# Optimization experiments

Hardware: AMD Instinct MI355X
Metric: run time of the kernel (lower is better)

Reference implementation:

```python
import jax, jax.numpy as jnp
import numpy as np
import math

B, N, D, H, FFN = 4, 2048, 512, 8, 2048
DK = D // H
EPS = 1e-5


def _layer_norm(x, g, b):
    mu = jnp.mean(x, axis=-1, keepdims=True)
    var = jnp.mean((x - mu) ** 2, axis=-1, keepdims=True)
    return (x - mu) * jax.lax.rsqrt(var + EPS) * g + b


def _rotate_half(x):
    h = x.shape[-1] // 2
    return jnp.concatenate([-x[..., h:], x[..., :h]], axis=-1)


def _rope(q, k, positions):
    # q, k: (B, H, N, DK); positions: (B, N) int
    inv_freq = 1.0 / (10000.0 ** (jnp.arange(0, DK, 2, dtype=jnp.float32) / DK))  # (DK/2,)
    ang = positions[:, None, :, None].astype(jnp.float32) * inv_freq  # (B,1,N,DK/2)
    cos = jnp.concatenate([jnp.cos(ang), jnp.cos(ang)], axis=-1)  # (B,1,N,DK)
    sin = jnp.concatenate([jnp.sin(ang), jnp.sin(ang)], axis=-1)
    q = q * cos + _rotate_half(q) * sin
    k = k * cos + _rotate_half(k) * sin
    return q, k


def setup_inputs() -> dict:
    key = jax.random.key(0)
    ks = jax.random.split(key, 16)
    s = 0.02
    x = jax.random.normal(ks[0], (B, N, D), dtype=jnp.float32)
    # backward-looking hop mask within jobs: random boolean with True diagonal
    m = jax.random.uniform(ks[1], (B, N, N)) < 0.1
    o2o_mask = m | jnp.eye(N, dtype=bool)[None]
    positions = jax.random.randint(ks[2], (B, N), 0, N)
    params = {
        'wq': jax.random.normal(ks[3], (D, D)) * s, 'bq': jnp.zeros((D,)),
        'wk': jax.random.normal(ks[4], (D, D)) * s, 'bk': jnp.zeros((D,)),
        'wv': jax.random.normal(ks[5], (D, D)) * s, 'bv': jnp.zeros((D,)),
        'wo': jax.random.normal(ks[6], (D, D)) * s, 'bo': jnp.zeros((D,)),
        'ln1_g': jnp.ones((D,)), 'ln1_b': jnp.zeros((D,)),
        'ln2_g': jnp.ones((D,)), 'ln2_b': jnp.zeros((D,)),
        'w1': jax.random.normal(ks[7], (D, FFN)) * s, 'b1': jnp.zeros((FFN,)),
        'w2': jax.random.normal(ks[8], (FFN, D)) * s, 'b2': jnp.zeros((D,)),
    }
    return {'x': x, 'o2o_mask': o2o_mask, 'positions': positions, **params}


def reference(x, o2o_mask, positions, wq, bq, wk, bk, wv, bv, wo, bo,
              ln1_g, ln1_b, ln2_g, ln2_b, w1, b1, w2, b2):
    residual = x
    xn = _layer_norm(x, ln1_g, ln1_b)
    q = (xn @ wq + bq).reshape(B, N, H, DK).transpose(0, 2, 1, 3)
    k = (xn @ wk + bk).reshape(B, N, H, DK).transpose(0, 2, 1, 3)
    v = (xn @ wv + bv).reshape(B, N, H, DK).transpose(0, 2, 1, 3)
    q, k = _rope(q, k, positions)
    scores = jnp.einsum('bhqd,bhkd->bhqk', q, k) / math.sqrt(DK)
    scores = jnp.where(o2o_mask[:, None], scores, -jnp.inf)
    attn = jax.nn.softmax(scores, axis=-1)
    attn = jnp.where(jnp.isnan(attn), 0.0, attn)  # fully-masked rows -> 0
    attn_out = jnp.einsum('bhqk,bhkd->bhqd', attn, v)
    attn_out = attn_out.transpose(0, 2, 1, 3).reshape(B, N, D)
    x = residual + (attn_out @ wo + bo)
    residual = x
    h = _layer_norm(x, ln2_g, ln2_b)
    h = jax.nn.relu(h @ w1 + b1) @ w2 + b2
    return residual + h
```

## Files before the change

kernel.cpp:

```cpp
#include <hip/hip_runtime.h>
#include <hip/hip_bf16.h>

typedef __attribute__((ext_vector_type(8))) __bf16 bf16x8;
typedef __attribute__((ext_vector_type(4))) __bf16 bf16x4;
typedef __attribute__((ext_vector_type(4))) float f32x4;

#define B_ 4
#define N_ 2048
#define D_ 512
#define H_ 8
#define DK_ 64
#define F_ 2048

__device__ __forceinline__ void async16(const __bf16* g, __bf16* l) {
  __builtin_amdgcn_global_load_lds((const __attribute__((address_space(1))) void*)g,
                                   (__attribute__((address_space(3))) void*)l, 16, 0, 0);
}

__global__ __launch_bounds__(256) void transpose_w(const float* __restrict__ in,
                                                   __bf16* __restrict__ out,
                                                   int K, int Nc) {
  __shared__ float t[64][65];
  const int k0 = blockIdx.x * 64, n0 = blockIdx.y * 64;
  const int c = threadIdx.x & 63, r4 = threadIdx.x >> 6;
#pragma unroll
  for (int p = 0; p < 16; p++) {
    int rr = p * 4 + r4;
    t[rr][c] = in[(size_t)(k0 + rr) * Nc + n0 + c];
  }
  __syncthreads();
#pragma unroll
  for (int p = 0; p < 16; p++) {
    int rr = p * 4 + r4;
    out[(size_t)(n0 + rr) * K + k0 + c] = (__bf16)t[c][rr];
  }
}

__global__ void concat_bias(const float* __restrict__ bq, const float* __restrict__ bk,
                            const float* __restrict__ bv, float* __restrict__ o) {
  int i = blockIdx.x * 256 + threadIdx.x;
  o[i] = (i < 512) ? bq[i] : (i < 1024) ? bk[i - 512] : bv[i - 1024];
}

__global__ __launch_bounds__(256) void build_bitmask(const int* __restrict__ mask,
                                                     unsigned long long* __restrict__ bm) {
  size_t t = (size_t)blockIdx.x * 256 + threadIdx.x;
  int m = mask[t];
  unsigned long long w = __ballot(m != 0);
  if ((threadIdx.x & 63) == 0) bm[t >> 6] = w;
}

__global__ __launch_bounds__(256) void ln_fwd(const float* __restrict__ x,
                                              const float* __restrict__ g,
                                              const float* __restrict__ b,
                                              __bf16* __restrict__ out) {
  int row = blockIdx.x * 4 + (threadIdx.x >> 6);
  int lane = threadIdx.x & 63;
  const float* xr = x + (size_t)row * D_ + lane * 8;
  float4 a0 = *(const float4*)xr;
  float4 a1 = *(const float4*)(xr + 4);
  float v[8] = {a0.x, a0.y, a0.z, a0.w, a1.x, a1.y, a1.z, a1.w};
  float s = 0.f;
#pragma unroll
  for (int i = 0; i < 8; i++) s += v[i];
#pragma unroll
  for (int off = 1; off < 64; off <<= 1) s += __shfl_xor(s, off);
  float mu = s * (1.f / D_);
  float q = 0.f;
#pragma unroll
  for (int i = 0; i < 8; i++) { float d = v[i] - mu; q += d * d; }
#pragma unroll
  for (int off = 1; off < 64; off <<= 1) q += __shfl_xor(q, off);
  float rs = rsqrtf(q * (1.f / D_) + 1e-5f);
  const float* gp = g + lane * 8;
  const float* bp = b + lane * 8;
  alignas(16) __bf16 o[8];
#pragma unroll
  for (int i = 0; i < 8; i++) o[i] = (__bf16)((v[i] - mu) * rs * gp[i] + bp[i]);
  *(bf16x8*)(out + (size_t)row * D_ + lane * 8) = *(bf16x8*)o;
}

__global__ __launch_bounds__(256) void rope_qk(const __bf16* __restrict__ qkv,
                                               const int* __restrict__ pos,
                                               __bf16* __restrict__ qo,
                                               __bf16* __restrict__ ko) {
  int t = blockIdx.x * 256 + threadIdx.x;
  int d = t & 31;
  int h = (t >> 5) & 7;
  int n = (t >> 8) & (N_ - 1);
  int b = t >> 19;
  const __bf16* base = qkv + (size_t)(b * N_ + n) * 1536 + h * 64 + d;
  float q1 = (float)base[0], q2 = (float)base[32];
  float k1 = (float)base[512], k2 = (float)base[544];
  float p = (float)pos[b * N_ + n];
  float inv = __expf(-(float)d * (9.210340371976184f / 32.f));
  float ang = p * inv;
  float sn, cs;
  sincosf(ang, &sn, &cs);
  size_t ob = ((size_t)(b * H_ + h) * N_ + n) * DK_ + d;
  qo[ob]      = (__bf16)(q1 * cs - q2 * sn);
  qo[ob + 32] = (__bf16)(q2 * cs + q1 * sn);
  ko[ob]      = (__bf16)(k1 * cs - k2 * sn);
  ko[ob + 32] = (__bf16)(k2 * cs + k1 * sn);
}

__global__ __launch_bounds__(256) void v_trans(const __bf16* __restrict__ qkv,
                                               __bf16* __restrict__ vt) {
  __shared__ __bf16 t[64][65];
  int n0 = blockIdx.x * 64, h = blockIdx.y, b = blockIdx.z;
  int c = threadIdx.x & 63, rr = threadIdx.x >> 6;
#pragma unroll
  for (int p = 0; p < 16; p++) {
    int i = p * 4 + rr;
    t[i][c] = qkv[(size_t)(b * N_ + n0 + i) * 1536 + 1024 + h * 64 + c];
  }
  __syncthreads();
  size_t ob = (size_t)(b * H_ + h) * DK_ * N_;
#pragma unroll
  for (int p = 0; p < 16; p++) {
    int dd = p * 4 + rr;
    vt[ob + (size_t)dd * N_ + n0 + c] = t[c][dd];
  }
}

template <int RELU, int OBF, int RES>
__global__ __launch_bounds__(256) void gemm_bt(const __bf16* __restrict__ A,
                                               const __bf16* __restrict__ Bt,
                                               const float* __restrict__ bias,
                                               const float* __restrict__ res,
                                               void* __restrict__ Cout,
                                               int M, int N, int K) {
  __shared__ __bf16 As[128 * 32];
  __shared__ __bf16 Bs[128 * 32];
  const int tid = threadIdx.x;
  const int lane = tid & 63;
  const int wave = tid >> 6;
  const int quad = lane >> 4;
  const int l16 = lane & 15;
  const int m0 = blockIdx.y * 128;
  const int n0 = blockIdx.x * 128;
  const int wm = (wave >> 1) * 64;
  const int wn = (wave & 1) * 64;
  f32x4 acc[4][4] = {};

  const int c0 = tid, c1 = tid + 256;
  const int ar0 = c0 >> 2, ak0 = (c0 & 3) * 8;
  const int ar1 = c1 >> 2, ak1 = (c1 & 3) * 8;

  for (int k0 = 0; k0 < K; k0 += 32) {
    async16(A + (size_t)(m0 + ar0) * K + k0 + ak0, As + c0 * 8);
    async16(A + (size_t)(m0 + ar1) * K + k0 + ak1, As + c1 * 8);
    async16(Bt + (size_t)(n0 + ar0) * K + k0 + ak0, Bs + c0 * 8);
    async16(Bt + (size_t)(n0 + ar1) * K + k0 + ak1, Bs + c1 * 8);
    __syncthreads();
    bf16x8 af[4], bf[4];
#pragma unroll
    for (int mi = 0; mi < 4; mi++)
      af[mi] = *(const bf16x8*)(As + (wm + mi * 16 + l16) * 32 + quad * 8);
#pragma unroll
    for (int ni = 0; ni < 4; ni++)
      bf[ni] = *(const bf16x8*)(Bs + (wn + ni * 16 + l16) * 32 + quad * 8);
#pragma unroll
    for (int mi = 0; mi < 4; mi++)
#pragma unroll
      for (int ni = 0; ni < 4; ni++)
        acc[mi][ni] = __builtin_amdgcn_mfma_f32_16x16x32_bf16(af[mi], bf[ni], acc[mi][ni], 0, 0, 0);
    __syncthreads();
  }
#pragma unroll
  for (int ni = 0; ni < 4; ni++) {
    const int col = n0 + wn + ni * 16 + l16;
    const float bv = bias[col];
#pragma unroll
    for (int mi = 0; mi < 4; mi++) {
#pragma unroll
      for (int r = 0; r < 4; r++) {
        const int row = m0 + wm + mi * 16 + quad * 4 + r;
        float v = acc[mi][ni][r] + bv;
        if (RES) v += res[(size_t)row * N + col];
        if (RELU) v = fmaxf(v, 0.f);
        if (OBF) ((__bf16*)Cout)[(size_t)row * N + col] = (__bf16)v;
        else     ((float*)Cout)[(size_t)row * N + col] = v;
      }
    }
  }
}

template <int RELU, int OBF, int RES>
__global__ __launch_bounds__(256) void gemm_bt64(const __bf16* __restrict__ A,
                                                 const __bf16* __restrict__ Bt,
                                                 const float* __restrict__ bias,
                                                 const float* __restrict__ res,
                                                 void* __restrict__ Cout,
                                                 int M, int N, int K) {
  __shared__ __bf16 As[128 * 32];
  __shared__ __bf16 Bs[64 * 32];
  const int tid = threadIdx.x;
  const int lane = tid & 63;
  const int wave = tid >> 6;
  const int quad = lane >> 4;
  const int l16 = lane & 15;
  const int m0 = blockIdx.y * 128;
  const int n0 = blockIdx.x * 64;
  const int wm = wave * 32;
  f32x4 acc[2][4] = {};

  const int ar0 = tid >> 2, ak0 = (tid & 3) * 8;

  for (int k0 = 0; k0 < K; k0 += 32) {
    async16(A + (size_t)(m0 + ar0) * K + k0 + ak0, As + tid * 8);
    async16(A + (size_t)(m0 + 64 + ar0) * K + k0 + ak0, As + (tid + 256) * 8);
    async16(Bt + (size_t)(n0 + ar0) * K + k0 + ak0, Bs + tid * 8);
    __syncthreads();
    bf16x8 af[2], bf[4];
#pragma unroll
    for (int mi = 0; mi < 2; mi++)
      af[mi] = *(const bf16x8*)(As + (wm + mi * 16 + l16) * 32 + quad * 8);
#pragma unroll
    for (int ni = 0; ni < 4; ni++)
      bf[ni] = *(const bf16x8*)(Bs + (ni * 16 + l16) * 32 + quad * 8);
#pragma unroll
    for (int mi = 0; mi < 2; mi++)
#pragma unroll
      for (int ni = 0; ni < 4; ni++)
        acc[mi][ni] = __builtin_amdgcn_mfma_f32_16x16x32_bf16(af[mi], bf[ni], acc[mi][ni], 0, 0, 0);
    __syncthreads();
  }
#pragma unroll
  for (int ni = 0; ni < 4; ni++) {
    const int col = n0 + ni * 16 + l16;
    const float bv = bias[col];
#pragma unroll
    for (int mi = 0; mi < 2; mi++) {
#pragma unroll
      for (int r = 0; r < 4; r++) {
        const int row = m0 + wm + mi * 16 + quad * 4 + r;
        float v = acc[mi][ni][r] + bv;
        if (RES) v += res[(size_t)row * N + col];
        if (RELU) v = fmaxf(v, 0.f);
        if (OBF) ((__bf16*)Cout)[(size_t)row * N + col] = (__bf16)v;
        else     ((float*)Cout)[(size_t)row * N + col] = v;
      }
    }
  }
}

__global__ __launch_bounds__(256, 2) void flash_attn(const __bf16* __restrict__ q,
                                                     const __bf16* __restrict__ k,
                                                     const __bf16* __restrict__ vt,
                                                     const unsigned long long* __restrict__ bm,
                                                     __bf16* __restrict__ out) {
  const int qt = blockIdx.x, h = blockIdx.y, b = blockIdx.z;
  const int tid = threadIdx.x;
  const int lane = tid & 63, wave = tid >> 6;
  const int quad = lane >> 4, l16 = lane & 15;
  __shared__ __bf16 Ks[2][64 * 64];
  __shared__ __bf16 Vs[2][64 * 64];
  __shared__ __bf16 P[4][2][16 * 68];
  const size_t bh = (size_t)b * H_ + h;
  const __bf16* qp = q + (bh * N_ + qt * 128 + wave * 32) * DK_;
  bf16x8 qf[2][2];
#pragma unroll
  for (int s = 0; s < 2; s++)
#pragma unroll
    for (int ks = 0; ks < 2; ks++) {
      qf[s][ks] = *(const bf16x8*)(qp + (s * 16 + l16) * DK_ + ks * 32 + quad * 8);
#pragma unroll
      for (int j = 0; j < 8; j++) qf[s][ks][j] = qf[s][ks][j] * (__bf16)0.125f;
    }
  const __bf16* kbase = k + bh * N_ * DK_;
  const __bf16* vbase = vt + bh * DK_ * N_;
  const int qrow0 = qt * 128 + wave * 32 + l16;
  const unsigned long long* bmr0 = bm + (size_t)(b * N_ + qrow0) * (N_ / 64);
  const unsigned long long* bmr1 = bmr0 + 16 * (N_ / 64);
  const int xo = l16 & 7;

  f32x4 oacc[2][4] = {};
  float lsum[2] = {0.f, 0.f};

  auto stage = [&](int kt, int buf) {
    const __bf16* kg = kbase + (size_t)kt * 64 * DK_;
    const __bf16* vg = vbase + kt * 64;
#pragma unroll
    for (int i = 0; i < 2; i++) {
      const int s = tid + i * 256;
      const int r = s >> 3;
      const int j = (s & 7) ^ (r & 7);
      async16(kg + r * DK_ + j * 8, Ks[buf] + s * 8);
      async16(vg + (size_t)r * N_ + j * 8, Vs[buf] + s * 8);
    }
  };

  stage(0, 0);
  __syncthreads();

  for (int kt = 0; kt < N_ / 64; kt++) {
    const int buf = kt & 1;
    if (kt + 1 < N_ / 64) stage(kt + 1, buf ^ 1);

    const unsigned long long mw0 = bmr0[kt] >> (quad * 4);
    const unsigned long long mw1 = bmr1[kt] >> (quad * 4);
#pragma unroll
    for (int ci = 0; ci < 4; ci++) {
      const int row = ci * 16 + l16;
      bf16x8 kf0 = *(const bf16x8*)(Ks[buf] + (row * 8 + (quad ^ xo)) * 8);
      bf16x8 kf1 = *(const bf16x8*)(Ks[buf] + (row * 8 + ((4 + quad) ^ xo)) * 8);
#pragma unroll
      for (int s = 0; s < 2; s++) {
        f32x4 a = {0.f, 0.f, 0.f, 0.f};
        a = __builtin_amdgcn_mfma_f32_16x16x32_bf16(kf0, qf[s][0], a, 0, 0, 0);
        a = __builtin_amdgcn_mfma_f32_16x16x32_bf16(kf1, qf[s][1], a, 0, 0, 0);
        const unsigned long long mw = s ? mw1 : mw0;
        bf16x4 pk;
#pragma unroll
        for (int r = 0; r < 4; r++) {
          float in = ((mw >> (ci * 16 + r)) & 1ull) ? a[r] : -1e30f;
          float p = __expf(in);
          lsum[s] += p;
          pk[r] = (__bf16)p;
        }
        *(bf16x4*)(&P[wave][s][0] + l16 * 68 + ci * 16 + quad * 4) = pk;
      }
    }
    bf16x8 pf[2][2];
#pragma unroll
    for (int s = 0; s < 2; s++) {
      pf[s][0] = *(const bf16x8*)(&P[wave][s][0] + l16 * 68 + quad * 8);
      pf[s][1] = *(const bf16x8*)(&P[wave][s][0] + l16 * 68 + 32 + quad * 8);
    }
#pragma unroll
    for (int ni = 0; ni < 4; ni++) {
      const int row = ni * 16 + l16;
      bf16x8 vf0 = *(const bf16x8*)(Vs[buf] + (row * 8 + (quad ^ xo)) * 8);
      bf16x8 vf1 = *(const bf16x8*)(Vs[buf] + (row * 8 + ((4 + quad) ^ xo)) * 8);
#pragma unroll
      for (int s = 0; s < 2; s++) {
        oacc[s][ni] = __builtin_amdgcn_mfma_f32_16x16x32_bf16(vf0, pf[s][0], oacc[s][ni], 0, 0, 0);
        oacc[s][ni] = __builtin_amdgcn_mfma_f32_16x16x32_bf16(vf1, pf[s][1], oacc[s][ni], 0, 0, 0);
      }
    }
    __syncthreads();
  }
#pragma unroll
  for (int s = 0; s < 2; s++) {
    lsum[s] += __shfl_xor(lsum[s], 16);
    lsum[s] += __shfl_xor(lsum[s], 32);
    const float inv_l = (lsum[s] > 0.f) ? 1.f / lsum[s] : 0.f;
#pragma unroll
    for (int ni = 0; ni < 4; ni++) {
      bf16x4 ov;
#pragma unroll
      for (int r = 0; r < 4; r++) ov[r] = (__bf16)(oacc[s][ni][r] * inv_l);
      *(bf16x4*)(out + ((size_t)b * N_ + qrow0 + s * 16) * D_ + h * DK_ + ni * 16 + quad * 4) = ov;
    }
  }
}

static constexpr size_t OFF_XN  = 0;
static constexpr size_t OFF_WT  = 8388608;
static constexpr size_t OFF_WO  = OFF_WT + 1572864;
static constexpr size_t OFF_W1  = OFF_WO + 524288;
static constexpr size_t OFF_W2  = OFF_W1 + 2097152;
static constexpr size_t OFF_BQ  = OFF_W2 + 2097152;
static constexpr size_t OFF_QKV = OFF_BQ + 6144;
static constexpr size_t OFF_QR  = OFF_QKV + 25165824;
static constexpr size_t OFF_KR  = OFF_QR + 8388608;
static constexpr size_t OFF_VT  = OFF_KR + 8388608;
static constexpr size_t OFF_AO  = OFF_VT + 8388608;
static constexpr size_t OFF_Y   = OFF_AO + 8388608;

extern "C" void kernel_launch(void* const* d_in, const int* in_sizes, int n_in,
                              void* d_out, int out_size, void* d_ws, size_t ws_size,
                              hipStream_t stream) {
  const float* x    = (const float*)d_in[0];
  const int*   mask = (const int*)d_in[1];
  const int*   pos  = (const int*)d_in[2];
  const float* wq   = (const float*)d_in[3];
  const float* bq   = (const float*)d_in[4];
  const float* wk   = (const float*)d_in[5];
  const float* bk   = (const float*)d_in[6];
  const float* wv   = (const float*)d_in[7];
  const float* bv   = (const float*)d_in[8];
  const float* wo   = (const float*)d_in[9];
  const float* bo   = (const float*)d_in[10];
  const float* ln1g = (const float*)d_in[11];
  const float* ln1b = (const float*)d_in[12];
  const float* ln2g = (const float*)d_in[13];
  const float* ln2b = (const float*)d_in[14];
  const float* w1   = (const float*)d_in[15];
  const float* b1   = (const float*)d_in[16];
  const float* w2   = (const float*)d_in[17];
  const float* b2   = (const float*)d_in[18];
  float* out = (float*)d_out;
  char* ws = (char*)d_ws;

  __bf16* xn    = (__bf16*)(ws + OFF_XN);
  __bf16* wqkvt = (__bf16*)(ws + OFF_WT);
  __bf16* wot   = (__bf16*)(ws + OFF_WO);
  __bf16* w1t   = (__bf16*)(ws + OFF_W1);
  __bf16* w2t   = (__bf16*)(ws + OFF_W2);
  float*  bqkv  = (float*)(ws + OFF_BQ);
  __bf16* qkv   = (__bf16*)(ws + OFF_QKV);
  __bf16* qr    = (__bf16*)(ws + OFF_QR);
  __bf16* kr    = (__bf16*)(ws + OFF_KR);
  __bf16* vt    = (__bf16*)(ws + OFF_VT);
  __bf16* attn  = (__bf16*)(ws + OFF_AO);
  float*  y     = (float*)(ws + OFF_Y);
  unsigned long long* bm = (unsigned long long*)(ws + OFF_Y);
  __bf16* hn    = xn;
  __bf16* h2    = qkv;

  dim3 b256(256);
  transpose_w<<<dim3(8, 8), b256, 0, stream>>>(wq, wqkvt, 512, 512);
  transpose_w<<<dim3(8, 8), b256, 0, stream>>>(wk, wqkvt + 512 * 512, 512, 512);
  transpose_w<<<dim3(8, 8), b256, 0, stream>>>(wv, wqkvt + 1024 * 512, 512, 512);
  transpose_w<<<dim3(8, 8), b256, 0, stream>>>(wo, wot, 512, 512);
  transpose_w<<<dim3(8, 32), b256, 0, stream>>>(w1, w1t, 512, 2048);
  transpose_w<<<dim3(32, 8), b256, 0, stream>>>(w2, w2t, 2048, 512);
  concat_bias<<<6, b256, 0, stream>>>(bq, bk, bv, bqkv);
  build_bitmask<<<65536, b256, 0, stream>>>(mask, bm);

  ln_fwd<<<2048, b256, 0, stream>>>(x, ln1g, ln1b, xn);
  gemm_bt<0, 1, 0><<<dim3(12, 64), b256, 0, stream>>>(xn, wqkvt, bqkv, nullptr, qkv, 8192, 1536, 512);
  rope_qk<<<8192, b256, 0, stream>>>(qkv, pos, qr, kr);
  v_trans<<<dim3(32, 8, 4), b256, 0, stream>>>(qkv, vt);

  flash_attn<<<dim3(16, 8, 4), b256, 0, stream>>>(qr, kr, vt, bm, attn);

  gemm_bt64<0, 0, 1><<<dim3(8, 64), b256, 0, stream>>>(attn, wot, bo, x, y, 8192, 512, 512);
  ln_fwd<<<2048, b256, 0, stream>>>(y, ln2g, ln2b, hn);
  gemm_bt<1, 1, 0><<<dim3(16, 64), b256, 0, stream>>>(hn, w1t, b1, nullptr, h2, 8192, 2048, 512);
  gemm_bt64<0, 0, 1><<<dim3(8, 64), b256, 0, stream>>>(h2, w2t, b2, y, out, 8192, 512, 2048);
}
```

Measured before the change: 391.4 us.

## Split attention KV range in two with combine kernel and MFMA row sums

New measurement: 417.6 us. 1.07x slower.

```diff
diff --git a/kernel.cpp b/kernel.cpp
--- a/kernel.cpp
+++ b/kernel.cpp
@@ -1,5 +1,6 @@
 #include <hip/hip_runtime.h>
 #include <hip/hip_bf16.h>
+#include <math.h>
 
 typedef __attribute__((ext_vector_type(8))) __bf16 bf16x8;
 typedef __attribute__((ext_vector_type(4))) __bf16 bf16x4;
@@ -245,12 +246,14 @@
   }
 }
 
-__global__ __launch_bounds__(256, 2) void flash_attn(const __bf16* __restrict__ q,
+__global__ __launch_bounds__(256, 3) void flash_attn(const __bf16* __restrict__ q,
                                                      const __bf16* __restrict__ k,
                                                      const __bf16* __restrict__ vt,
                                                      const unsigned long long* __restrict__ bm,
-                                                     __bf16* __restrict__ out) {
-  const int qt = blockIdx.x, h = blockIdx.y, b = blockIdx.z;
+                                                     __bf16* __restrict__ po,
+                                                     float* __restrict__ lsg) {
+  const int qt = blockIdx.x, h = blockIdx.y;
+  const int b = blockIdx.z >> 1, half = blockIdx.z & 1;
   const int tid = threadIdx.x;
   const int lane = tid & 63, wave = tid >> 6;
   const int quad = lane >> 4, l16 = lane & 15;
@@ -259,15 +262,20 @@
   __shared__ __bf16 P[4][2][16 * 68];
   const size_t bh = (size_t)b * H_ + h;
   const __bf16* qp = q + (bh * N_ + qt * 128 + wave * 32) * DK_;
+  const float qscale = 0.125f * 1.44269504f;
   bf16x8 qf[2][2];
 #pragma unroll
   for (int s = 0; s < 2; s++)
 #pragma unroll
     for (int ks = 0; ks < 2; ks++) {
-      qf[s][ks] = *(const bf16x8*)(qp + (s * 16 + l16) * DK_ + ks * 32 + quad * 8);
-#pragma unroll
-      for (int j = 0; j < 8; j++) qf[s][ks][j] = qf[s][ks][j] * (__bf16)0.125f;
-    }
+      bf16x8 raw = *(const bf16x8*)(qp + (s * 16 + l16) * DK_ + ks * 32 + quad * 8);
+#pragma unroll
+      for (int j = 0; j < 8; j++) qf[s][ks][j] = (__bf16)((float)raw[j] * qscale);
+    }
+  bf16x8 onesf;
+#pragma unroll
+  for (int j = 0; j < 8; j++) onesf[j] = (__bf16)1.0f;
+
   const __bf16* kbase = k + bh * N_ * DK_;
   const __bf16* vbase = vt + bh * DK_ * N_;
   const int qrow0 = qt * 128 + wave * 32 + l16;
@@ -275,8 +283,19 @@
   const unsigned long long* bmr1 = bmr0 + 16 * (N_ / 64);
   const int xo = l16 & 7;
 
+  const __bf16* kA[2], * kB[2], * vA[2], * vB[2];
+#pragma unroll
+  for (int bf = 0; bf < 2; bf++) {
+    kA[bf] = Ks[bf] + (l16 * 8 + (quad ^ xo)) * 8;
+    kB[bf] = Ks[bf] + (l16 * 8 + ((4 + quad) ^ xo)) * 8;
+    vA[bf] = Vs[bf] + (l16 * 8 + (quad ^ xo)) * 8;
+    vB[bf] = Vs[bf] + (l16 * 8 + ((4 + quad) ^ xo)) * 8;
+  }
+  __bf16* Pw[2] = {&P[wave][0][0] + l16 * 68 + quad * 4, &P[wave][1][0] + l16 * 68 + quad * 4};
+  const __bf16* Pr[2] = {&P[wave][0][0] + l16 * 68 + quad * 8, &P[wave][1][0] + l16 * 68 + quad * 8};
+
   f32x4 oacc[2][4] = {};
-  float lsum[2] = {0.f, 0.f};
+  f32x4 lacc[2] = {};
 
   auto stage = [&](int kt, int buf) {
     const __bf16* kg = kbase + (size_t)kt * 64 * DK_;
@@ -291,48 +310,53 @@
     }
   };
 
-  stage(0, 0);
+  const int kt0 = half * 16;
+  stage(kt0, 0);
+  unsigned long long nm0 = bmr0[kt0], nm1 = bmr1[kt0];
   __syncthreads();
 
-  for (int kt = 0; kt < N_ / 64; kt++) {
-    const int buf = kt & 1;
-    if (kt + 1 < N_ / 64) stage(kt + 1, buf ^ 1);
-
-    const unsigned long long mw0 = bmr0[kt] >> (quad * 4);
-    const unsigned long long mw1 = bmr1[kt] >> (quad * 4);
+  for (int it = 0; it < 16; it++) {
+    const int kt = kt0 + it;
+    const int buf = it & 1;
+    if (it + 1 < 16) stage(kt + 1, buf ^ 1);
+    const unsigned long long mw0 = nm0 >> (quad * 4);
+    const unsigned long long mw1 = nm1 >> (quad * 4);
+    if (it + 1 < 16) { nm0 = bmr0[kt + 1]; nm1 = bmr1[kt + 1]; }
+
 #pragma unroll
     for (int ci = 0; ci < 4; ci++) {
-      const int row = ci * 16 + l16;
-      bf16x8 kf0 = *(const bf16x8*)(Ks[buf] + (row * 8 + (quad ^ xo)) * 8);
-      bf16x8 kf1 = *(const bf16x8*)(Ks[buf] + (row * 8 + ((4 + quad) ^ xo)) * 8);
+      bf16x8 kf0 = *(const bf16x8*)(kA[buf] + ci * 1024);
+      bf16x8 kf1 = *(const bf16x8*)(kB[buf] + ci * 1024);
 #pragma unroll
       for (int s = 0; s < 2; s++) {
         f32x4 a = {0.f, 0.f, 0.f, 0.f};
         a = __builtin_amdgcn_mfma_f32_16x16x32_bf16(kf0, qf[s][0], a, 0, 0, 0);
         a = __builtin_amdgcn_mfma_f32_16x16x32_bf16(kf1, qf[s][1], a, 0, 0, 0);
-        const unsigned long long mw = s ? mw1 : mw0;
+        const unsigned nib = (unsigned)((s ? mw1 : mw0) >> (ci * 16)) & 15u;
         bf16x4 pk;
 #pragma unroll
         for (int r = 0; r < 4; r++) {
-          float in = ((mw >> (ci * 16 + r)) & 1ull) ? a[r] : -1e30f;
-          float p = __expf(in);
-          lsum[s] += p;
-          pk[r] = (__bf16)p;
+          float in = (nib & (1u << r)) ? a[r] : -1e30f;
+          pk[r] = (__bf16)exp2f(in);
         }
-        *(bf16x4*)(&P[wave][s][0] + l16 * 68 + ci * 16 + quad * 4) = pk;
+        *(bf16x4*)(Pw[s] + ci * 16) = pk;
       }
     }
     bf16x8 pf[2][2];
 #pragma unroll
     for (int s = 0; s < 2; s++) {
-      pf[s][0] = *(const bf16x8*)(&P[wave][s][0] + l16 * 68 + quad * 8);
-      pf[s][1] = *(const bf16x8*)(&P[wave][s][0] + l16 * 68 + 32 + quad * 8);
+      pf[s][0] = *(const bf16x8*)(Pr[s]);
+      pf[s][1] = *(const bf16x8*)(Pr[s] + 32);
+    }
+#pragma unroll
+    for (int s = 0; s < 2; s++) {
+      lacc[s] = __builtin_amdgcn_mfma_f32_16x16x32_bf16(onesf, pf[s][0], lacc[s], 0, 0, 0);
+      lacc[s] = __builtin_amdgcn_mfma_f32_16x16x32_bf16(onesf, pf[s][1], lacc[s], 0, 0, 0);
     }
 #pragma unroll
     for (int ni = 0; ni < 4; ni++) {
-      const int row = ni * 16 + l16;
-      bf16x8 vf0 = *(const bf16x8*)(Vs[buf] + (row * 8 + (quad ^ xo)) * 8);
-      bf16x8 vf1 = *(const bf16x8*)(Vs[buf] + (row * 8 + ((4 + quad) ^ xo)) * 8);
+      bf16x8 vf0 = *(const bf16x8*)(vA[buf] + ni * 1024);
+      bf16x8 vf1 = *(const bf16x8*)(vB[buf] + ni * 1024);
 #pragma unroll
       for (int s = 0; s < 2; s++) {
         oacc[s][ni] = __builtin_amdgcn_mfma_f32_16x16x32_bf16(vf0, pf[s][0], oacc[s][ni], 0, 0, 0);
@@ -341,19 +365,41 @@
     }
     __syncthreads();
   }
+  const size_t BND = (size_t)B_ * N_ * D_;
 #pragma unroll
   for (int s = 0; s < 2; s++) {
-    lsum[s] += __shfl_xor(lsum[s], 16);
-    lsum[s] += __shfl_xor(lsum[s], 32);
-    const float inv_l = (lsum[s] > 0.f) ? 1.f / lsum[s] : 0.f;
+    const int qrow = qrow0 + s * 16;
+    if (quad == 0) lsg[(size_t)half * (B_ * H_ * N_) + bh * N_ + qrow] = lacc[s][0];
 #pragma unroll
     for (int ni = 0; ni < 4; ni++) {
       bf16x4 ov;
 #pragma unroll
-      for (int r = 0; r < 4; r++) ov[r] = (__bf16)(oacc[s][ni][r] * inv_l);
-      *(bf16x4*)(out + ((size_t)b * N_ + qrow0 + s * 16) * D_ + h * DK_ + ni * 16 + quad * 4) = ov;
-    }
-  }
+      for (int r = 0; r < 4; r++) ov[r] = (__bf16)oacc[s][ni][r];
+      *(bf16x4*)(po + half * BND + ((size_t)b * N_ + qrow) * D_ + h * DK_ + ni * 16 + quad * 4) = ov;
+    }
+  }
+}
+
+__global__ __launch_bounds__(256) void attn_combine(const __bf16* __restrict__ po,
+                                                    const float* __restrict__ lsg,
+                                                    __bf16* __restrict__ outp) {
+  const size_t BND = (size_t)B_ * N_ * D_;
+  const int BHN = B_ * H_ * N_;
+  int t = blockIdx.x * 256 + threadIdx.x;
+  int d4 = t & 127;
+  int row = t >> 7;
+  int hh = d4 >> 4;
+  int b = row >> 11, n = row & (N_ - 1);
+  float l0 = lsg[(b * H_ + hh) * N_ + n];
+  float l1 = lsg[BHN + (b * H_ + hh) * N_ + n];
+  float l = l0 + l1;
+  float inv = (l > 0.f) ? 1.f / l : 0.f;
+  bf16x4 a = *(const bf16x4*)(po + (size_t)row * D_ + d4 * 4);
+  bf16x4 c = *(const bf16x4*)(po + BND + (size_t)row * D_ + d4 * 4);
+  bf16x4 o;
+#pragma unroll
+  for (int r = 0; r < 4; r++) o[r] = (__bf16)(((float)a[r] + (float)c[r]) * inv);
+  *(bf16x4*)(outp + (size_t)row * D_ + d4 * 4) = o;
 }
 
 static constexpr size_t OFF_XN  = 0;
@@ -407,6 +453,8 @@
   __bf16* attn  = (__bf16*)(ws + OFF_AO);
   float*  y     = (float*)(ws + OFF_Y);
   unsigned long long* bm = (unsigned long long*)(ws + OFF_Y);
+  __bf16* po    = (__bf16*)(ws + OFF_QKV);
+  float*  lsg   = (float*)(ws + OFF_XN);
   __bf16* hn    = xn;
   __bf16* h2    = qkv;
 
@@ -425,7 +473,8 @@
   rope_qk<<<8192, b256, 0, stream>>>(qkv, pos, qr, kr);
   v_trans<<<dim3(32, 8, 4), b256, 0, stream>>>(qkv, vt);
 
-  flash_attn<<<dim3(16, 8, 4), b256, 0, stream>>>(qr, kr, vt, bm, attn);
+  flash_attn<<<dim3(16, 8, 8), b256, 0, stream>>>(qr, kr, vt, bm, po, lsg);
+  attn_combine<<<4096, b256, 0, stream>>>(po, lsg, attn);
 
   gemm_bt64<0, 0, 1><<<dim3(8, 64), b256, 0, stream>>>(attn, wot, bo, x, y, 8192, 512, 512);
   ln_fwd<<<2048, b256, 0, stream>>>(y, ln2g, ln2b, hn);
```
